# Kernel tuning notes

Hardware: AMD Instinct MI355X
Metric: run time of the kernel (lower is better)

Reference implementation:

```python
import jax, jax.numpy as jnp
import numpy as np

N = 50000
T = 6
E = 800000
F_IN = 64
HID = 64
HEADS = 4
NEG_SLOPE = 0.2
BN_EPS = 1e-5


def _gat_layer(x, src, dst, W, att_src, att_dst, bias, concat):
    # x: [N, Fin]; W: [Fin, H*C]; att_*: [H, C]; src/dst: [E+N] (self loops appended)
    n = x.shape[0]
    H, C = att_src.shape
    xl = (x @ W).reshape(n, H, C)                     # [N, H, C]
    a_src = jnp.sum(xl * att_src[None], axis=-1)      # [N, H]
    a_dst = jnp.sum(xl * att_dst[None], axis=-1)      # [N, H]
    e = jax.nn.leaky_relu(a_src[src] + a_dst[dst], NEG_SLOPE)  # [E', H]
    # segment softmax over destination nodes (every node has a self loop)
    m = jax.ops.segment_max(e, dst, num_segments=n)
    ex = jnp.exp(e - m[dst])
    s = jax.ops.segment_sum(ex, dst, num_segments=n)
    alpha = ex / (s[dst] + 1e-16)                     # [E', H]
    msg = alpha[:, :, None] * xl[src]                 # [E', H, C]
    out = jax.ops.segment_sum(msg, dst, num_segments=n)  # [N, H, C]
    if concat:
        out = out.reshape(n, H * C)
    else:
        out = out.mean(axis=1)
    return out + bias


def _forward(x_seq, edge_index, W1, as1, ad1, b1, W2, as2, ad2, b2,
             cw1, cb1, g1, be1, cw2, cb2, g2, be2, lw1, lb1, lw2, lb2):
    n = x_seq.shape[1]
    self_loop = jnp.arange(n, dtype=edge_index.dtype)
    src = jnp.concatenate([edge_index[0], self_loop])
    dst = jnp.concatenate([edge_index[1], self_loop])

    def per_t(x):
        h = _gat_layer(x, src, dst, W1, as1, ad1, b1, concat=True)
        h = jax.nn.elu(h)
        h = _gat_layer(h, src, dst, W2, as2, ad2, b2, concat=False)
        h = jax.nn.elu(h)
        return h                                      # [N, HID]

    temporal = jax.vmap(per_t)(x_seq)                 # [T, N, HID]
    temporal = jnp.transpose(temporal, (1, 2, 0))     # [N, HID, T]

    def conv_bn_relu(t, cw, cb, g, be):
        y = jax.lax.conv_general_dilated(
            t, cw, window_strides=(1,), padding=[(1, 1)],
            dimension_numbers=('NCH', 'OIH', 'NCH')) + cb[None, :, None]
        # BatchNorm1d in eval mode, running_mean=0, running_var=1
        y = y * (g / jnp.sqrt(1.0 + BN_EPS))[None, :, None] + be[None, :, None]
        return jax.nn.relu(y)

    t = conv_bn_relu(temporal, cw1, cb1, g1, be1)
    t = conv_bn_relu(t, cw2, cb2, g2, be2)
    pooled = t.mean(axis=-1)                          # adaptive avg pool -> [N, HID]
    h = jax.nn.relu(pooled @ lw1 + lb1)
    logits = h @ lw2 + lb2                            # [N, 1]
    return logits


def setup_inputs() -> dict:
    key = jax.random.key(0)
    ks = jax.random.split(key, 20)
    C1 = HID // HEADS  # 16
    s = 0.1
    return {
        'x_seq': jax.random.normal(ks[0], (T, N, F_IN), jnp.float32),
        'edge_index': jax.random.randint(ks[1], (2, E), 0, N, jnp.int32),
        'W1': jax.random.normal(ks[2], (F_IN, HEADS * C1), jnp.float32) * s,
        'as1': jax.random.normal(ks[3], (HEADS, C1), jnp.float32) * s,
        'ad1': jax.random.normal(ks[4], (HEADS, C1), jnp.float32) * s,
        'b1': jnp.zeros((HEADS * C1,), jnp.float32),
        'W2': jax.random.normal(ks[5], (HID, HEADS * HID), jnp.float32) * s,
        'as2': jax.random.normal(ks[6], (HEADS, HID), jnp.float32) * s,
        'ad2': jax.random.normal(ks[7], (HEADS, HID), jnp.float32) * s,
        'b2': jnp.zeros((HID,), jnp.float32),
        'cw1': jax.random.normal(ks[8], (HID, HID, 3), jnp.float32) * s,
        'cb1': jnp.zeros((HID,), jnp.float32),
        'g1': jnp.ones((HID,), jnp.float32),
        'be1': jnp.zeros((HID,), jnp.float32),
        'cw2': jax.random.normal(ks[9], (HID, HID, 3), jnp.float32) * s,
        'cb2': jnp.zeros((HID,), jnp.float32),
        'g2': jnp.ones((HID,), jnp.float32),
        'be2': jnp.zeros((HID,), jnp.float32),
        'lw1': jax.random.normal(ks[10], (HID, HID // 2), jnp.float32) * s,
        'lb1': jnp.zeros((HID // 2,), jnp.float32),
        'lw2': jax.random.normal(ks[11], (HID // 2, 1), jnp.float32) * s,
        'lb2': jnp.zeros((1,), jnp.float32),
    }


def reference(x_seq, edge_index, W1, as1, ad1, b1, W2, as2, ad2, b2,
              cw1, cb1, g1, be1, cw2, cb2, g2, be2, lw1, lb1, lw2, lb2):
    return _forward(x_seq, edge_index, W1, as1, ad1, b1, W2, as2, ad2, b2,
                    cw1, cb1, g1, be1, cw2, cb2, g2, be2, lw1, lb1, lw2, lb2)
```

## Files before the change

kernel.cpp:

```cpp
#include <hip/hip_runtime.h>
#include <math.h>

#define NN 50000
#define EE 800000
#define TT 6
#define SS (EE+NN)

__device__ __forceinline__ float lrelu(float x){ return x > 0.f ? x : 0.2f*x; }
__device__ __forceinline__ float eluf(float x){ return x > 0.f ? x : expm1f(x); }

__global__ void k_init_counts(int* __restrict__ c){
  int i = blockIdx.x*256 + threadIdx.x;
  if (i < NN) c[i] = 1;
}

__global__ void k_hist(const int* __restrict__ dst, int* __restrict__ c){
  int i = blockIdx.x*256 + threadIdx.x;
  if (i < EE) atomicAdd(&c[dst[i]], 1);
}

__global__ void k_scanA(const int* __restrict__ cnt, int* __restrict__ excl,
                        int* __restrict__ bsum){
  __shared__ int sh[1024];
  int tid = threadIdx.x;
  int i = blockIdx.x*1024 + tid;
  int v = (i < NN) ? cnt[i] : 0;
  int x = v;
  sh[tid] = x; __syncthreads();
  for (int off = 1; off < 1024; off <<= 1){
    int y = (tid >= off) ? sh[tid - off] : 0;
    __syncthreads();
    x += y; sh[tid] = x; __syncthreads();
  }
  if (i < NN) excl[i] = x - v;
  if (tid == 1023) bsum[blockIdx.x] = x;
}

__global__ void k_scanB(int* __restrict__ bsum, int nb){
  if (threadIdx.x == 0){
    int run = 0;
    for (int b = 0; b < nb; ++b){ int t = bsum[b]; bsum[b] = run; run += t; }
  }
}

__global__ void k_scanC(const int* __restrict__ excl, const int* __restrict__ bsum,
                        int* __restrict__ rowptr, int* __restrict__ cursor){
  int i = blockIdx.x*1024 + threadIdx.x;
  if (i < NN){
    int v = excl[i] + bsum[blockIdx.x];
    rowptr[i] = v; cursor[i] = v;
  }
  if (i == 0) rowptr[NN] = SS;
}

__global__ void k_scatter(const int* __restrict__ ei, int* __restrict__ cursor,
                          int* __restrict__ csr, int* __restrict__ dstOf){
  int i = blockIdx.x*256 + threadIdx.x;
  if (i < EE){
    int d = ei[EE + i];
    int p = atomicAdd(&cursor[d], 1);
    csr[p] = ei[i];
    dstOf[p] = d;
  } else if (i < SS){
    int v = i - EE;
    int p = atomicAdd(&cursor[v], 1);
    csr[p] = v;
    dstOf[p] = v;
  }
}

__global__ void k_prep(const float* __restrict__ W1, const float* __restrict__ as1,
                       const float* __restrict__ ad1,
                       const float* __restrict__ W2, const float* __restrict__ as2,
                       const float* __restrict__ ad2,
                       const float* __restrict__ cw1, const float* __restrict__ cw2,
                       const float* __restrict__ lw1,
                       float* __restrict__ Was1, float* __restrict__ Wad1,
                       float* __restrict__ Wat2, float* __restrict__ Wb,
                       float4* __restrict__ wq1, float4* __restrict__ wq2,
                       float* __restrict__ lw1t){
  int tid = threadIdx.x;
  int k = tid >> 2, h = tid & 3;
  float s1 = 0.f, d1 = 0.f, s2 = 0.f, d2 = 0.f;
  for (int c = 0; c < 16; ++c){
    float w = W1[k*64 + h*16 + c];
    s1 += w * as1[h*16 + c];
    d1 += w * ad1[h*16 + c];
  }
  for (int c = 0; c < 64; ++c){
    float w = W2[k*256 + h*64 + c];
    s2 += w * as2[h*64 + c];
    d2 += w * ad2[h*64 + c];
  }
  Was1[k*4+h] = s1; Wad1[k*4+h] = d1;
  Wat2[k*8 + h] = s2; Wat2[k*8 + 4 + h] = d2;
  for (int idx = tid; idx < 256*64; idx += 256){
    int kf = idx >> 6, c = idx & 63;
    int hh = kf >> 6, kk = kf & 63;
    Wb[idx] = W2[kk*256 + hh*64 + c];
  }
  for (int idx = tid; idx < 64*64; idx += 256){
    int i = idx >> 6, o = idx & 63;
    wq1[idx] = make_float4(cw1[o*192+i*3], cw1[o*192+i*3+1], cw1[o*192+i*3+2], 0.f);
    wq2[idx] = make_float4(cw2[o*192+i*3], cw2[o*192+i*3+1], cw2[o*192+i*3+2], 0.f);
  }
  for (int idx = tid; idx < 32*64; idx += 256){
    int j = idx >> 6, kk = idx & 63;
    lw1t[idx] = lw1[kk*32 + j];
  }
}

__global__ __launch_bounds__(256) void k_gemm_att1(const float* __restrict__ A,
                            const float* __restrict__ W,
                            const float* __restrict__ Was, const float* __restrict__ Wad,
                            float* __restrict__ Xl, float* __restrict__ a_src,
                            float* __restrict__ a_dst){
  __shared__ float At[64][16];
  int tid = threadIdx.x;
  int r0 = blockIdx.x * 16;
  {
    const float4* A4 = (const float4*)(A + (size_t)r0*64);
    float4 v = A4[tid];
    int r = tid >> 4, k4 = (tid & 15) << 2;
    At[k4+0][r] = v.x; At[k4+1][r] = v.y;
    At[k4+2][r] = v.z; At[k4+3][r] = v.w;
  }
  __syncthreads();
  int col = tid & 63;
  int rbase = (tid >> 6) << 2;
  float acc0=0.f, acc1=0.f, acc2=0.f, acc3=0.f;
  for (int k = 0; k < 64; ++k){
    float w = W[k*64 + col];
    float4 a4 = *(const float4*)&At[k][rbase];
    acc0 += a4.x*w; acc1 += a4.y*w; acc2 += a4.z*w; acc3 += a4.w*w;
  }
  Xl[(size_t)(r0+rbase+0)*64 + col] = acc0;
  Xl[(size_t)(r0+rbase+1)*64 + col] = acc1;
  Xl[(size_t)(r0+rbase+2)*64 + col] = acc2;
  Xl[(size_t)(r0+rbase+3)*64 + col] = acc3;
  if (tid < 128){
    int r = tid >> 3, jx = tid & 7;
    int h = jx & 3;
    const float* Wv = (jx < 4) ? Was : Wad;
    float a = 0.f;
    for (int k = 0; k < 64; ++k) a += At[k][r] * Wv[k*4 + h];
    if (jx < 4) a_src[(r0 + r)*4 + h] = a;
    else        a_dst[(r0 + r)*4 + h] = a;
  }
}

__global__ __launch_bounds__(256) void k_edge1(const int* __restrict__ csr,
                        const int* __restrict__ dstOf,
                        const float* __restrict__ a_src, const float* __restrict__ a_dst,
                        float* __restrict__ peh){
  int k = blockIdx.x*256 + threadIdx.x;
  if (k >= SS) return;
  int sn = csr[k], dn = dstOf[k];
  float4 as = ((const float4*)a_src)[sn];
  float4 ad = ((const float4*)a_dst)[dn];
  peh[k]                 = __expf(lrelu(as.x+ad.x));
  peh[(size_t)SS + k]    = __expf(lrelu(as.y+ad.y));
  peh[2*(size_t)SS + k]  = __expf(lrelu(as.z+ad.z));
  peh[3*(size_t)SS + k]  = __expf(lrelu(as.w+ad.w));
}

__global__ __launch_bounds__(256) void k_edge2(const int* __restrict__ csr,
                        const int* __restrict__ dstOf,
                        const float* __restrict__ a_src, const float* __restrict__ a_dst,
                        float4* __restrict__ pe4){
  int k = blockIdx.x*256 + threadIdx.x;
  if (k >= SS) return;
  int sn = csr[k], dn = dstOf[k];
  float4 as = ((const float4*)a_src)[sn];
  float4 ad = ((const float4*)a_dst)[dn];
  pe4[k] = make_float4(__expf(lrelu(as.x+ad.x)), __expf(lrelu(as.y+ad.y)),
                       __expf(lrelu(as.z+ad.z)), __expf(lrelu(as.w+ad.w)));
}

__global__ __launch_bounds__(256) void k_agg1(
                       const float* __restrict__ xl, const float* __restrict__ peh,
                       const float* __restrict__ b1, const float* __restrict__ Wat2,
                       const int* __restrict__ rowptr, const int* __restrict__ csr,
                       float* __restrict__ h1,
                       float* __restrict__ a_src2, float* __restrict__ a_dst2){
  int lane = threadIdx.x & 63;
  int wid  = __builtin_amdgcn_readfirstlane(threadIdx.x >> 6);
  int n = blockIdx.x*4 + wid;
  int h = lane >> 4;
  const float* __restrict__ ph = peh + (size_t)h*SS;
  int rs = rowptr[n], re = rowptr[n+1];
  float s = 0.f, acc = 0.f;
  int j = rs;
  for (; j + 4 <= re; j += 4){
    int sn0=csr[j], sn1=csr[j+1], sn2=csr[j+2], sn3=csr[j+3];
    float p0=ph[j], p1=ph[j+1], p2=ph[j+2], p3=ph[j+3];
    float x0=xl[(size_t)sn0*64+lane], x1=xl[(size_t)sn1*64+lane];
    float x2=xl[(size_t)sn2*64+lane], x3=xl[(size_t)sn3*64+lane];
    s += p0; acc += p0*x0;
    s += p1; acc += p1*x1;
    s += p2; acc += p2*x2;
    s += p3; acc += p3*x3;
  }
  for (; j < re; ++j){
    int sn = csr[j];
    float p = ph[j];
    float x = xl[(size_t)sn*64 + lane];
    s += p; acc += p*x;
  }
  float hv = eluf(acc/(s + 1e-16f) + b1[lane]);
  h1[(size_t)n*64 + lane] = hv;
  float4 wA = ((const float4*)Wat2)[lane*2];
  float4 wB = ((const float4*)Wat2)[lane*2 + 1];
  float p[8];
  p[0]=hv*wA.x; p[1]=hv*wA.y; p[2]=hv*wA.z; p[3]=hv*wA.w;
  p[4]=hv*wB.x; p[5]=hv*wB.y; p[6]=hv*wB.z; p[7]=hv*wB.w;
#pragma unroll
  for (int off = 32; off >= 1; off >>= 1){
#pragma unroll
    for (int q = 0; q < 8; ++q) p[q] += __shfl_xor(p[q], off);
  }
  if (lane == 0){
    ((float4*)a_src2)[n] = make_float4(p[0],p[1],p[2],p[3]);
    ((float4*)a_dst2)[n] = make_float4(p[4],p[5],p[6],p[7]);
  }
}

__global__ __launch_bounds__(256) void k_agg2(
                       const float* __restrict__ h1, const float4* __restrict__ pe4,
                       const int* __restrict__ rowptr, const int* __restrict__ csr,
                       float* __restrict__ agg){
  int lane = threadIdx.x & 63;
  int wid  = __builtin_amdgcn_readfirstlane(threadIdx.x >> 6);
  int n = blockIdx.x*4 + wid;
  int rs = rowptr[n], re = rowptr[n+1];
  float s0=0.f,s1=0.f,s2=0.f,s3=0.f;
  float g0=0.f,g1=0.f,g2=0.f,g3=0.f;
  int j = rs;
  for (; j + 4 <= re; j += 4){
    int sa=csr[j], sb=csr[j+1], sc=csr[j+2], sd=csr[j+3];
    float4 pa = pe4[j];
    float4 pb = pe4[j+1];
    float4 pc = pe4[j+2];
    float4 pd = pe4[j+3];
    float xa = h1[(size_t)sa*64 + lane];
    float xb = h1[(size_t)sb*64 + lane];
    float xc = h1[(size_t)sc*64 + lane];
    float xd = h1[(size_t)sd*64 + lane];
    s0 += pa.x+pb.x+pc.x+pd.x; g0 += pa.x*xa + pb.x*xb + pc.x*xc + pd.x*xd;
    s1 += pa.y+pb.y+pc.y+pd.y; g1 += pa.y*xa + pb.y*xb + pc.y*xc + pd.y*xd;
    s2 += pa.z+pb.z+pc.z+pd.z; g2 += pa.z*xa + pb.z*xb + pc.z*xc + pd.z*xd;
    s3 += pa.w+pb.w+pc.w+pd.w; g3 += pa.w*xa + pb.w*xb + pc.w*xc + pd.w*xd;
  }
  for (; j < re; ++j){
    int sn = csr[j];
    float4 pv = pe4[j];
    float x = h1[(size_t)sn*64 + lane];
    s0 += pv.x; g0 += pv.x*x;
    s1 += pv.y; g1 += pv.y*x;
    s2 += pv.z; g2 += pv.z*x;
    s3 += pv.w; g3 += pv.w*x;
  }
  size_t base = (size_t)n*256 + lane;
  agg[base      ] = g0/(s0 + 1e-16f);
  agg[base +  64] = g1/(s1 + 1e-16f);
  agg[base + 128] = g2/(s2 + 1e-16f);
  agg[base + 192] = g3/(s3 + 1e-16f);
}

__global__ __launch_bounds__(256) void k_out2(const float* __restrict__ agg,
                                              const float* __restrict__ Wb,
                                              const float* __restrict__ b2,
                                              float* __restrict__ ht){
  __shared__ float A[64*257];
  int tid = threadIdx.x;
  int lane = tid & 63;
  int w = __builtin_amdgcn_readfirstlane(tid >> 6);
  int r0 = blockIdx.x * 64;
  for (int jj = 0; jj < 64; ++jj){
    int m = jj*256 + tid;
    int row = m >> 8, k = m & 255;
    int rsrc = r0 + row; if (rsrc >= NN) rsrc = NN-1;
    A[row*257 + k] = agg[(size_t)rsrc*256 + k];
  }
  __syncthreads();
  const float* __restrict__ Wbw = Wb + w*16;
  float acc[16];
#pragma unroll
  for (int jq = 0; jq < 16; ++jq) acc[jq] = 0.f;
  const float* Ar = A + lane*257;
#pragma unroll 8
  for (int k = 0; k < 256; ++k){
    float a = Ar[k];
#pragma unroll
    for (int jq = 0; jq < 16; ++jq) acc[jq] += a * Wbw[(k<<6) + jq];
  }
  __syncthreads();
#pragma unroll
  for (int jq = 0; jq < 16; ++jq){
    int c = w*16 + jq;
    A[lane*65 + c] = eluf(0.25f*acc[jq] + b2[c]);
  }
  __syncthreads();
  for (int jj = 0; jj < 16; ++jj){
    int m = jj*256 + tid;
    int row = m >> 6, c = m & 63;
    int rdst = r0 + row;
    if (rdst < NN) ht[(size_t)rdst*64 + c] = A[row*65 + c];
  }
}

__global__ __launch_bounds__(512) void k_conv(const float* __restrict__ htb,
    const float4* __restrict__ wq1, const float* __restrict__ cb1,
    const float* __restrict__ g1,   const float* __restrict__ be1,
    const float4* __restrict__ wq2, const float* __restrict__ cb2,
    const float* __restrict__ g2,   const float* __restrict__ be2,
    const float* __restrict__ lw1t, const float* __restrict__ lb1,
    const float* __restrict__ lw2,  const float* __restrict__ lb2,
    float* __restrict__ out){
  __shared__ float X[64*384];
  __shared__ float pool_lds[64*64];
  __shared__ float outp[8][64];
  int tid  = threadIdx.x;
  int lane = tid & 63;
  int w    = __builtin_amdgcn_readfirstlane(tid >> 6);
  int n0 = blockIdx.x*64;
  int n  = n0 + lane;
  int ob = w*8;

#pragma unroll
  for (int it = 0; it < 8; ++it){
    int p  = it*512 + tid;
    int ch = p & 63, ns = p >> 6;
    int nsrc = n0 + ns; if (nsrc >= NN) nsrc = NN-1;
    float xv[6];
#pragma unroll
    for (int t = 0; t < 6; ++t) xv[t] = htb[((size_t)t*NN + nsrc)*64 + ch];
#pragma unroll
    for (int t = 0; t < 6; ++t) X[ch*384 + t*64 + ns] = xv[t];
  }
  __syncthreads();

  float acc[8][6];
#pragma unroll
  for (int q = 0; q < 8; ++q){
    float c = cb1[ob+q];
#pragma unroll
    for (int t = 0; t < 6; ++t) acc[q][t] = c;
  }
  for (int i = 0; i < 64; ++i){
    const float* xp = X + i*384 + lane;
    float x1 = xp[0], x2 = xp[64], x3 = xp[128];
    float x4 = xp[192], x5 = xp[256], x6 = xp[320];
    const float4* wrow = wq1 + (i<<6) + ob;
#pragma unroll
    for (int q = 0; q < 8; ++q){
      float4 wv = wrow[q];
      acc[q][0] += wv.y*x1 + wv.z*x2;
      acc[q][1] += wv.x*x1 + wv.y*x2 + wv.z*x3;
      acc[q][2] += wv.x*x2 + wv.y*x3 + wv.z*x4;
      acc[q][3] += wv.x*x3 + wv.y*x4 + wv.z*x5;
      acc[q][4] += wv.x*x4 + wv.y*x5 + wv.z*x6;
      acc[q][5] += wv.x*x5 + wv.y*x6;
    }
  }
  __syncthreads();
#pragma unroll
  for (int q = 0; q < 8; ++q){
    float bns = g1[ob+q]*rsqrtf(1.f + 1e-5f), be = be1[ob+q];
    float* xp = X + (ob+q)*384 + lane;
#pragma unroll
    for (int t = 0; t < 6; ++t) xp[t*64] = fmaxf(acc[q][t]*bns + be, 0.f);
  }
  __syncthreads();

#pragma unroll
  for (int q = 0; q < 8; ++q){
    float c = cb2[ob+q];
#pragma unroll
    for (int t = 0; t < 6; ++t) acc[q][t] = c;
  }
  for (int i = 0; i < 64; ++i){
    const float* xp = X + i*384 + lane;
    float x1 = xp[0], x2 = xp[64], x3 = xp[128];
    float x4 = xp[192], x5 = xp[256], x6 = xp[320];
    const float4* wrow = wq2 + (i<<6) + ob;
#pragma unroll
    for (int q = 0; q < 8; ++q){
      float4 wv = wrow[q];
      acc[q][0] += wv.y*x1 + wv.z*x2;
      acc[q][1] += wv.x*x1 + wv.y*x2 + wv.z*x3;
      acc[q][2] += wv.x*x2 + wv.y*x3 + wv.z*x4;
      acc[q][3] += wv.x*x3 + wv.y*x4 + wv.z*x5;
      acc[q][4] += wv.x*x4 + wv.y*x5 + wv.z*x6;
      acc[q][5] += wv.x*x5 + wv.y*x6;
    }
  }
#pragma unroll
  for (int q = 0; q < 8; ++q){
    float bns = g2[ob+q]*rsqrtf(1.f + 1e-5f), be = be2[ob+q];
    float pooled = 0.f;
#pragma unroll
    for (int t = 0; t < 6; ++t) pooled += fmaxf(acc[q][t]*bns + be, 0.f);
    pool_lds[(ob+q)*64 + lane] = pooled*(1.f/6.f);
  }
  __syncthreads();

  {
    float po = 0.f;
#pragma unroll
    for (int jj = 0; jj < 4; ++jj){
      int jdx = w*4 + jj;
      float hj = lb1[jdx];
      const float* lw = lw1t + jdx*64;
#pragma unroll 8
      for (int k = 0; k < 64; ++k) hj += pool_lds[k*64 + lane] * lw[k];
      po += fmaxf(hj, 0.f) * lw2[jdx];
    }
    outp[w][lane] = po;
  }
  __syncthreads();
  if (w == 0 && n < NN){
    float r = lb2[0];
#pragma unroll
    for (int q = 0; q < 8; ++q) r += outp[q][lane];
    out[n] = r;
  }
}

extern "C" void kernel_launch(void* const* d_in, const int* in_sizes, int n_in,
                              void* d_out, int out_size, void* d_ws, size_t ws_size,
                              hipStream_t stream) {
  const float* x_seq = (const float*)d_in[0];
  const int*   ei    = (const int*)  d_in[1];
  const float* W1  = (const float*)d_in[2];
  const float* as1 = (const float*)d_in[3];
  const float* ad1 = (const float*)d_in[4];
  const float* b1  = (const float*)d_in[5];
  const float* W2  = (const float*)d_in[6];
  const float* as2 = (const float*)d_in[7];
  const float* ad2 = (const float*)d_in[8];
  const float* b2  = (const float*)d_in[9];
  const float* cw1 = (const float*)d_in[10];
  const float* cb1 = (const float*)d_in[11];
  const float* g1  = (const float*)d_in[12];
  const float* be1 = (const float*)d_in[13];
  const float* cw2 = (const float*)d_in[14];
  const float* cb2 = (const float*)d_in[15];
  const float* g2  = (const float*)d_in[16];
  const float* be2 = (const float*)d_in[17];
  const float* lw1 = (const float*)d_in[18];
  const float* lb1 = (const float*)d_in[19];
  const float* lw2 = (const float*)d_in[20];
  const float* lb2 = (const float*)d_in[21];
  float* out = (float*)d_out;

  char* wp = (char*)d_ws;
  auto alloc = [&](size_t bytes) -> char* {
    char* p = wp; wp += (bytes + 255) & ~(size_t)255; return p;
  };
  int*   counts = (int*)  alloc(NN*sizeof(int));
  int*   excl   = (int*)  alloc(NN*sizeof(int));
  int*   bsum   = (int*)  alloc(64*sizeof(int));
  int*   rowptr = (int*)  alloc((NN+1)*sizeof(int));
  int*   cursor = (int*)  alloc(NN*sizeof(int));
  int*   csr    = (int*)  alloc((size_t)SS*sizeof(int));
  int*   dstOf  = (int*)  alloc((size_t)SS*sizeof(int));
  float* peh    = (float*)alloc((size_t)4*SS*sizeof(float));
  float4* pe4   = (float4*)alloc((size_t)SS*sizeof(float4));
  float* a_src1 = (float*)alloc((size_t)NN*4*sizeof(float));
  float* a_dst1 = (float*)alloc((size_t)NN*4*sizeof(float));
  float* a_src2 = (float*)alloc((size_t)NN*4*sizeof(float));
  float* a_dst2 = (float*)alloc((size_t)NN*4*sizeof(float));
  float* h1     = (float*)alloc((size_t)NN*64*sizeof(float));
  float* agg    = (float*)alloc((size_t)NN*256*sizeof(float));
  float* xl1    = agg;
  float* htb    = (float*)alloc((size_t)TT*NN*64*sizeof(float));
  float* Was1 = (float*)alloc(256*sizeof(float));
  float* Wad1 = (float*)alloc(256*sizeof(float));
  float* Wat2 = (float*)alloc(64*8*sizeof(float));
  float* Wb   = (float*)alloc(256*64*sizeof(float));
  float4* wq1 = (float4*)alloc(64*64*sizeof(float4));
  float4* wq2 = (float4*)alloc(64*64*sizeof(float4));
  float* lw1t = (float*)alloc(32*64*sizeof(float));

  const int NBSCAN = (NN + 1023)/1024;
  k_init_counts<<<(NN+255)/256, 256, 0, stream>>>(counts);
  k_hist<<<(EE+255)/256, 256, 0, stream>>>(ei + EE, counts);
  k_scanA<<<NBSCAN, 1024, 0, stream>>>(counts, excl, bsum);
  k_scanB<<<1, 64, 0, stream>>>(bsum, NBSCAN);
  k_scanC<<<NBSCAN, 1024, 0, stream>>>(excl, bsum, rowptr, cursor);
  k_scatter<<<(SS+255)/256, 256, 0, stream>>>(ei, cursor, csr, dstOf);
  k_prep<<<1, 256, 0, stream>>>(W1, as1, ad1, W2, as2, ad2, cw1, cw2, lw1,
                                Was1, Wad1, Wat2, Wb, wq1, wq2, lw1t);

  const int NEDGE = (SS + 255)/256;
  const int NOUT2 = (NN + 63)/64;
  for (int t = 0; t < TT; ++t){
    const float* xt = x_seq + (size_t)t*NN*64;
    k_gemm_att1<<<NN/16, 256, 0, stream>>>(xt, W1, Was1, Wad1, xl1, a_src1, a_dst1);
    k_edge1<<<NEDGE, 256, 0, stream>>>(csr, dstOf, a_src1, a_dst1, peh);
    k_agg1<<<NN/4, 256, 0, stream>>>(xl1, peh, b1, Wat2, rowptr, csr,
                                     h1, a_src2, a_dst2);
    k_edge2<<<NEDGE, 256, 0, stream>>>(csr, dstOf, a_src2, a_dst2, pe4);
    k_agg2<<<NN/4, 256, 0, stream>>>(h1, pe4, rowptr, csr, agg);
    k_out2<<<NOUT2, 256, 0, stream>>>(agg, Wb, b2, htb + (size_t)t*NN*64);
  }
  k_conv<<<(NN+63)/64, 512, 0, stream>>>(htb, wq1, cb1, g1, be1, wq2, cb2, g2, be2,
                                         lw1t, lb1, lw2, lb2, out);
}
```

Baseline: 1.440 ms.

## Split conv kernel into smaller-tile conv and separate MLP head kernel

```diff
diff --git a/kernel.cpp b/kernel.cpp
--- a/kernel.cpp
+++ b/kernel.cpp
@@ -309,34 +309,31 @@
   }
 }
 
-__global__ __launch_bounds__(512) void k_conv(const float* __restrict__ htb,
+__global__ __launch_bounds__(256) void k_conv(const float* __restrict__ htb,
     const float4* __restrict__ wq1, const float* __restrict__ cb1,
     const float* __restrict__ g1,   const float* __restrict__ be1,
     const float4* __restrict__ wq2, const float* __restrict__ cb2,
     const float* __restrict__ g2,   const float* __restrict__ be2,
-    const float* __restrict__ lw1t, const float* __restrict__ lb1,
-    const float* __restrict__ lw2,  const float* __restrict__ lb2,
-    float* __restrict__ out){
-  __shared__ float X[64*384];
-  __shared__ float pool_lds[64*64];
-  __shared__ float outp[8][64];
+    float* __restrict__ pooledG){
+  __shared__ float X[64*199];
   int tid  = threadIdx.x;
   int lane = tid & 63;
   int w    = __builtin_amdgcn_readfirstlane(tid >> 6);
-  int n0 = blockIdx.x*64;
-  int n  = n0 + lane;
-  int ob = w*8;
+  int nn   = lane & 31;
+  int ch2  = lane >> 5;
+  int n0 = blockIdx.x*32;
+  int n  = n0 + nn;
+  int ob = w*16 + ch2*8;
 
 #pragma unroll
   for (int it = 0; it < 8; ++it){
-    int p  = it*512 + tid;
-    int ch = p & 63, ns = p >> 6;
+    int ns = it*4 + w;
     int nsrc = n0 + ns; if (nsrc >= NN) nsrc = NN-1;
     float xv[6];
 #pragma unroll
-    for (int t = 0; t < 6; ++t) xv[t] = htb[((size_t)t*NN + nsrc)*64 + ch];
-#pragma unroll
-    for (int t = 0; t < 6; ++t) X[ch*384 + t*64 + ns] = xv[t];
+    for (int t = 0; t < 6; ++t) xv[t] = htb[((size_t)t*NN + nsrc)*64 + lane];
+#pragma unroll
+    for (int t = 0; t < 6; ++t) X[lane*199 + t*33 + ns] = xv[t];
   }
   __syncthreads();
 
@@ -348,9 +345,9 @@
     for (int t = 0; t < 6; ++t) acc[q][t] = c;
   }
   for (int i = 0; i < 64; ++i){
-    const float* xp = X + i*384 + lane;
-    float x1 = xp[0], x2 = xp[64], x3 = xp[128];
-    float x4 = xp[192], x5 = xp[256], x6 = xp[320];
+    const float* xp = X + i*199 + nn;
+    float x1 = xp[0], x2 = xp[33], x3 = xp[66];
+    float x4 = xp[99], x5 = xp[132], x6 = xp[165];
     const float4* wrow = wq1 + (i<<6) + ob;
 #pragma unroll
     for (int q = 0; q < 8; ++q){
@@ -367,9 +364,9 @@
 #pragma unroll
   for (int q = 0; q < 8; ++q){
     float bns = g1[ob+q]*rsqrtf(1.f + 1e-5f), be = be1[ob+q];
-    float* xp = X + (ob+q)*384 + lane;
-#pragma unroll
-    for (int t = 0; t < 6; ++t) xp[t*64] = fmaxf(acc[q][t]*bns + be, 0.f);
+    float* xp = X + (ob+q)*199 + nn;
+#pragma unroll
+    for (int t = 0; t < 6; ++t) xp[t*33] = fmaxf(acc[q][t]*bns + be, 0.f);
   }
   __syncthreads();
 
@@ -380,9 +377,9 @@
     for (int t = 0; t < 6; ++t) acc[q][t] = c;
   }
   for (int i = 0; i < 64; ++i){
-    const float* xp = X + i*384 + lane;
-    float x1 = xp[0], x2 = xp[64], x3 = xp[128];
-    float x4 = xp[192], x5 = xp[256], x6 = xp[320];
+    const float* xp = X + i*199 + nn;
+    float x1 = xp[0], x2 = xp[33], x3 = xp[66];
+    float x4 = xp[99], x5 = xp[132], x6 = xp[165];
     const float4* wrow = wq2 + (i<<6) + ob;
 #pragma unroll
     for (int q = 0; q < 8; ++q){
@@ -395,36 +392,37 @@
       acc[q][5] += wv.x*x5 + wv.y*x6;
     }
   }
-#pragma unroll
-  for (int q = 0; q < 8; ++q){
-    float bns = g2[ob+q]*rsqrtf(1.f + 1e-5f), be = be2[ob+q];
-    float pooled = 0.f;
-#pragma unroll
-    for (int t = 0; t < 6; ++t) pooled += fmaxf(acc[q][t]*bns + be, 0.f);
-    pool_lds[(ob+q)*64 + lane] = pooled*(1.f/6.f);
-  }
-  __syncthreads();
-
-  {
-    float po = 0.f;
-#pragma unroll
-    for (int jj = 0; jj < 4; ++jj){
-      int jdx = w*4 + jj;
-      float hj = lb1[jdx];
-      const float* lw = lw1t + jdx*64;
-#pragma unroll 8
-      for (int k = 0; k < 64; ++k) hj += pool_lds[k*64 + lane] * lw[k];
-      po += fmaxf(hj, 0.f) * lw2[jdx];
+  if (n < NN){
+#pragma unroll
+    for (int q = 0; q < 8; ++q){
+      float bns = g2[ob+q]*rsqrtf(1.f + 1e-5f), be = be2[ob+q];
+      float pooled = 0.f;
+#pragma unroll
+      for (int t = 0; t < 6; ++t) pooled += fmaxf(acc[q][t]*bns + be, 0.f);
+      pooledG[(size_t)(ob+q)*NN + n] = pooled*(1.f/6.f);
     }
-    outp[w][lane] = po;
-  }
-  __syncthreads();
-  if (w == 0 && n < NN){
-    float r = lb2[0];
-#pragma unroll
-    for (int q = 0; q < 8; ++q) r += outp[q][lane];
-    out[n] = r;
-  }
+  }
+}
+
+__global__ __launch_bounds__(256) void k_mlp(const float* __restrict__ pooledG,
+    const float* __restrict__ lw1t, const float* __restrict__ lb1,
+    const float* __restrict__ lw2,  const float* __restrict__ lb2,
+    float* __restrict__ out){
+  int lane = threadIdx.x & 63;
+  int w = __builtin_amdgcn_readfirstlane(threadIdx.x >> 6);
+  int n = (blockIdx.x*4 + w)*64 + lane;
+  int nc = (n < NN) ? n : (NN-1);
+  float p[64];
+#pragma unroll 16
+  for (int o = 0; o < 64; ++o) p[o] = pooledG[(size_t)o*NN + nc];
+  float po = 0.f;
+  for (int j = 0; j < 32; ++j){
+    float hj = lb1[j];
+#pragma unroll 16
+    for (int k = 0; k < 64; ++k) hj += p[k] * lw1t[j*64 + k];
+    po += fmaxf(hj, 0.f) * lw2[j];
+  }
+  if (n < NN) out[n] = po + lb2[0];
 }
 
 extern "C" void kernel_launch(void* const* d_in, const int* in_sizes, int n_in,
@@ -475,6 +473,7 @@
   float* agg    = (float*)alloc((size_t)NN*256*sizeof(float));
   float* xl1    = agg;
   float* htb    = (float*)alloc((size_t)TT*NN*64*sizeof(float));
+  float* pooledG= (float*)alloc((size_t)64*NN*sizeof(float));
   float* Was1 = (float*)alloc(256*sizeof(float));
   float* Wad1 = (float*)alloc(256*sizeof(float));
   float* Wat2 = (float*)alloc(64*8*sizeof(float));
@@ -505,6 +504,7 @@
     k_agg2<<<NN/4, 256, 0, stream>>>(h1, pe4, rowptr, csr, agg);
     k_out2<<<NOUT2, 256, 0, stream>>>(agg, Wb, b2, htb + (size_t)t*NN*64);
   }
-  k_conv<<<(NN+63)/64, 512, 0, stream>>>(htb, wq1, cb1, g1, be1, wq2, cb2, g2, be2,
-                                         lw1t, lb1, lw2, lb2, out);
-}
+  k_conv<<<(NN+31)/32, 256, 0, stream>>>(htb, wq1, cb1, g1, be1, wq2, cb2, g2, be2,
+                                         pooledG);
+  k_mlp<<<(NN+255)/256, 256, 0, stream>>>(pooledG, lw1t, lb1, lw2, lb2, out);
+}
```

Measured after the change: 1.408 ms. -2.3%, faster.
